# Kernel optimization log

Hardware: AMD Instinct MI355X
Metric: run time of the kernel (lower is better)

The kernel has to match this reference:

```python
import jax, jax.numpy as jnp
import numpy as np

SEQ_LEN = 2048
D_MODEL = 1024
K = 32
B = 16
CP = K * (K + 1) // 2  # 528


def _spectral_filters(seq_len: int, k: int) -> np.ndarray:
    # Hankel matrix Z_ij = 2 / ((i+j)^3 - (i+j)), 1-indexed
    e = np.arange(1, seq_len + 1, dtype=np.float64)
    ipj = e[:, None] + e[None, :]
    Z = 2.0 / (ipj ** 3 - ipj)
    sigma, phi = np.linalg.eigh(Z)
    sk = np.clip(sigma[-k:], 1e-9, None)
    return (phi[:, -k:] * sk ** 0.25).astype(np.float32)


# static upper-triangular index pattern and sqrt(2) off-diagonal scaling
_IU0, _IU1 = np.triu_indices(K)
_SCALE = np.where(_IU0 == _IU1, 1.0, np.sqrt(2.0)).astype(np.float32)


def setup_inputs() -> dict:
    key = jax.random.key(0)
    ks = jax.random.split(key, 8)
    filters = jnp.asarray(_spectral_filters(SEQ_LEN, K))
    x = jax.random.normal(ks[0], (B, SEQ_LEN, D_MODEL), dtype=jnp.float32)
    pre_w = jax.random.normal(ks[1], (SEQ_LEN, D_MODEL), dtype=jnp.float32) / np.sqrt(D_MODEL)
    pre_b = jnp.zeros((SEQ_LEN,), dtype=jnp.float32)
    qp_w = jax.random.normal(ks[2], (CP, K), dtype=jnp.float32) / np.sqrt(K)
    qp_b = jnp.zeros((CP,), dtype=jnp.float32)
    o_w = jax.random.normal(ks[3], (D_MODEL, CP), dtype=jnp.float32) / np.sqrt(CP)
    o_b = jnp.zeros((D_MODEL,), dtype=jnp.float32)
    decay = jnp.ones((SEQ_LEN,), dtype=jnp.float32)
    return {
        'x': x,
        'pre_w': pre_w, 'pre_b': pre_b,
        'q_filters': filters,          # learnable copy
        'k_filters': filters,          # fixed buffer copy
        'qp_w': qp_w, 'qp_b': qp_b,
        'o_w': o_w, 'o_b': o_b,
        'decay': decay,
    }


def reference(x, pre_w, pre_b, q_filters, k_filters, qp_w, qp_b, o_w, o_b, decay):
    # pre_proj: (B,T,d_model) -> (B,T,seq_len)
    x_proj = x @ pre_w.T + pre_b
    # spectral projections onto top-K filters: (B,T,K)
    Q = jnp.einsum('bti,ik->btk', x_proj, q_filters)
    Q = Q @ qp_w.T + qp_b                      # (B,T,CP)
    V = jnp.einsum('bti,ik->btk', x_proj, k_filters)
    # symmetric outer product compressed to upper triangle, off-diag * sqrt(2)
    iu0 = jnp.asarray(_IU0)
    iu1 = jnp.asarray(_IU1)
    scale = jnp.asarray(_SCALE)
    Z = V[..., iu0] * V[..., iu1] * scale      # (B,T,CP), avoids (B,T,K,K)
    Z = Z * decay[None, :, None]
    H = jnp.cumsum(Z, axis=1)                  # causal state accumulation
    Y = Q * H
    return Y @ o_w.T + o_b                     # (B,T,d_model)
```

## Files before the change

### kernel.cpp

```cpp
#include <hip/hip_runtime.h>
#include <hip/hip_bf16.h>
#include <math.h>

#define T_SEQ   2048
#define DM      1024
#define KF      32
#define BATCH   16
#define CPDIM   528
#define KPAD    544
#define YSTR    552
#define MROWS   (BATCH * T_SEQ)
#define NCHUNK  32
#define TCHUNK  64

typedef __bf16 bf16x8 __attribute__((ext_vector_type(8)));
typedef float f32x4 __attribute__((ext_vector_type(4)));
typedef unsigned uint2v __attribute__((ext_vector_type(2)));

__device__ __forceinline__ unsigned packsplit(float v) {
  unsigned u = __float_as_uint(v);
  unsigned h = (u + 0x7fffu + ((u >> 16) & 1u)) & 0xffff0000u;
  float rr = v - __uint_as_float(h);
  return h | (__float_as_uint(rr) >> 16);
}

__device__ __forceinline__ unsigned short f2bf(float f) {
  unsigned u = __float_as_uint(f);
  return (unsigned short)((u + 0x7fffu + ((u >> 16) & 1u)) >> 16);
}
__device__ __forceinline__ float bf2f(unsigned short h) {
  return __uint_as_float((unsigned)h << 16);
}

__device__ __forceinline__ void gload16(const void* g, void* l) {
  __builtin_amdgcn_global_load_lds(
      (const __attribute__((address_space(1))) unsigned*)g,
      (__attribute__((address_space(3))) unsigned*)l, 16, 0, 0);
}

__global__ __launch_bounds__(256) void k_fold_part(const float* __restrict__ pre_w,
                                                   const float* __restrict__ qf,
                                                   const float* __restrict__ kfil,
                                                   float* __restrict__ Wp) {
  const int sc = blockIdx.x;
  const int it = blockIdx.y;
  const int s0 = sc * 64, i0 = it * 64;
  const int tid = threadIdx.x;
  __shared__ float fs[64][64];
  __shared__ float ps[64][64];
  for (int idx = tid; idx < 4096; idx += 256) {
    const int s = idx >> 6, c = idx & 63;
    fs[s][c] = (c < KF) ? qf[(s0 + s) * KF + c] : kfil[(s0 + s) * KF + c - KF];
    ps[s][c] = pre_w[(size_t)(s0 + s) * DM + i0 + c];
  }
  __syncthreads();
  const int i = tid & 63;
  const int kb = tid >> 6;
  float acc[16] = {};
  for (int s = 0; s < 64; ++s) {
    const float pv = ps[s][i];
    const float4 f0 = *reinterpret_cast<const float4*>(&fs[s][kb * 16 + 0]);
    const float4 f1 = *reinterpret_cast<const float4*>(&fs[s][kb * 16 + 4]);
    const float4 f2 = *reinterpret_cast<const float4*>(&fs[s][kb * 16 + 8]);
    const float4 f3 = *reinterpret_cast<const float4*>(&fs[s][kb * 16 + 12]);
    acc[0]  = fmaf(pv, f0.x, acc[0]);  acc[1]  = fmaf(pv, f0.y, acc[1]);
    acc[2]  = fmaf(pv, f0.z, acc[2]);  acc[3]  = fmaf(pv, f0.w, acc[3]);
    acc[4]  = fmaf(pv, f1.x, acc[4]);  acc[5]  = fmaf(pv, f1.y, acc[5]);
    acc[6]  = fmaf(pv, f1.z, acc[6]);  acc[7]  = fmaf(pv, f1.w, acc[7]);
    acc[8]  = fmaf(pv, f2.x, acc[8]);  acc[9]  = fmaf(pv, f2.y, acc[9]);
    acc[10] = fmaf(pv, f2.z, acc[10]); acc[11] = fmaf(pv, f2.w, acc[11]);
    acc[12] = fmaf(pv, f3.x, acc[12]); acc[13] = fmaf(pv, f3.y, acc[13]);
    acc[14] = fmaf(pv, f3.z, acc[14]); acc[15] = fmaf(pv, f3.w, acc[15]);
  }
#pragma unroll
  for (int j = 0; j < 16; ++j)
    Wp[((size_t)sc * 64 + kb * 16 + j) * DM + i0 + i] = acc[j];
}

__global__ __launch_bounds__(256) void k_foldred_bias(const float* __restrict__ Wp,
                                                      const float* __restrict__ pre_b,
                                                      const float* __restrict__ qf,
                                                      const float* __restrict__ kfil,
                                                      unsigned short* __restrict__ Wt_hi,
                                                      unsigned short* __restrict__ Wt_lo,
                                                      float* __restrict__ bias64) {
  if (blockIdx.x == 256) {
    __shared__ float part[4][64];
    const int k = threadIdx.x & 63;
    const int q = threadIdx.x >> 6;
    float acc = 0.f;
    for (int s = q * 512; s < (q + 1) * 512; ++s) {
      const float fv = (k < KF) ? qf[s * KF + k] : kfil[s * KF + k - KF];
      acc = fmaf(pre_b[s], fv, acc);
    }
    part[q][k] = acc;
    __syncthreads();
    if (threadIdx.x < 64)
      bias64[threadIdx.x] = part[0][k] + part[1][k] + part[2][k] + part[3][k];
    return;
  }
  const int idx = blockIdx.x * 256 + threadIdx.x;
  float acc = 0.f;
#pragma unroll
  for (int sc = 0; sc < NCHUNK; ++sc)
    acc += Wp[(size_t)sc * 64 * DM + idx];
  const unsigned pk = packsplit(acc);
  Wt_hi[idx] = (unsigned short)(pk >> 16);
  Wt_lo[idx] = (unsigned short)(pk & 0xffffu);
}

__global__ __launch_bounds__(512) void k_q0v_cs(const float* __restrict__ x,
                                                const unsigned short* __restrict__ Wt_hi,
                                                const unsigned short* __restrict__ Wt_lo,
                                                const float* __restrict__ bias64,
                                                const float* __restrict__ decay,
                                                float* __restrict__ Q0V,
                                                float* __restrict__ S) {
  __shared__ float Xs[3][64 * 32];
  __shared__ unsigned short Wh[3][64 * 32];
  __shared__ unsigned short Wl[3][64 * 32];
  __shared__ float vs2[64 * 32];
  __shared__ float dec2[64];
  const int tid = threadIdx.x;
  const int m0 = blockIdx.x * 64;
  const int ph = blockIdx.x & 31;
  const int w = tid >> 6, l = tid & 63;
  const int g = l >> 4, r = l & 15;
  const int wr = w & 3, wh = w >> 2;

  f32x4 acc[2] = {};

  auto kcol = [&](int i) { return ((i + ph) & 31) * 32; };

  auto stage = [&](int buf, int k0) {
    {
      const int row = tid >> 3, sl = tid & 7;
      const int col4 = (sl ^ (row & 7)) * 4;
      gload16(&x[(size_t)(m0 + row) * DM + k0 + col4], &Xs[buf][tid * 4]);
    }
    {
      const int c2 = tid & 255;
      const int row = c2 >> 2, sl = c2 & 3;
      const int colh = (sl ^ ((row >> 1) & 3)) * 8;
      unsigned short* dst = (tid < 256) ? &Wh[buf][c2 * 8] : &Wl[buf][c2 * 8];
      const unsigned short* src = (tid < 256) ? &Wt_hi[(size_t)row * DM + k0 + colh]
                                              : &Wt_lo[(size_t)row * DM + k0 + colh];
      gload16(src, dst);
    }
  };

  auto compute = [&](int cur) {
    const int arow = wr * 16 + r;
    const int sx = (2 * g) ^ (arow & 7);
    const int sy = (2 * g + 1) ^ (arow & 7);
    const f32x4 pX = *reinterpret_cast<const f32x4*>(&Xs[cur][arow * 32 + sx * 4]);
    const f32x4 pY = *reinterpret_cast<const f32x4*>(&Xs[cur][arow * 32 + sy * 4]);
    unsigned pk[8];
#pragma unroll
    for (int e = 0; e < 4; ++e) { pk[e] = packsplit(pX[e]); pk[4 + e] = packsplit(pY[e]); }
    union { unsigned u[4]; bf16x8 v; } ah, al;
#pragma unroll
    for (int j = 0; j < 4; ++j) {
      ah.u[j] = (pk[2 * j] >> 16) | (pk[2 * j + 1] & 0xffff0000u);
      al.u[j] = (pk[2 * j] & 0xffffu) | (pk[2 * j + 1] << 16);
    }
    bf16x8 bh[2], bl[2];
#pragma unroll
    for (int nb = 0; nb < 2; ++nb) {
      const int brow = (wh * 2 + nb) * 16 + r;
      const int bs = g ^ ((brow >> 1) & 3);
      const int off = brow * 32 + bs * 8;
      bh[nb] = *reinterpret_cast<const bf16x8*>(&Wh[cur][off]);
      bl[nb] = *reinterpret_cast<const bf16x8*>(&Wl[cur][off]);
    }
#pragma unroll
    for (int nb = 0; nb < 2; ++nb) {
      acc[nb] = __builtin_amdgcn_mfma_f32_16x16x32_bf16(bh[nb], ah.v, acc[nb], 0, 0, 0);
      acc[nb] = __builtin_amdgcn_mfma_f32_16x16x32_bf16(bh[nb], al.v, acc[nb], 0, 0, 0);
      acc[nb] = __builtin_amdgcn_mfma_f32_16x16x32_bf16(bl[nb], ah.v, acc[nb], 0, 0, 0);
    }
  };

  if (tid < 64) dec2[tid] = decay[(m0 & 2047) + tid];

  stage(0, kcol(0));
  stage(1, kcol(1));

  for (int base = 0; base < 30; base += 3) {
#pragma unroll
    for (int sub = 0; sub < 3; ++sub) {
      const int it = base + sub;
      asm volatile("s_waitcnt vmcnt(2)" ::: "memory");
      __builtin_amdgcn_s_barrier();
      __builtin_amdgcn_sched_barrier(0);
      stage((sub + 2) % 3, kcol(it + 2));
      compute(sub);
    }
  }
  asm volatile("s_waitcnt vmcnt(2)" ::: "memory");
  __builtin_amdgcn_s_barrier();
  __builtin_amdgcn_sched_barrier(0);
  compute(0);
  asm volatile("s_waitcnt vmcnt(0)" ::: "memory");
  __builtin_amdgcn_s_barrier();
  __builtin_amdgcn_sched_barrier(0);
  compute(1);

  const int trow = wr * 16 + r;
  const int row_o = m0 + trow;
#pragma unroll
  for (int nb = 0; nb < 2; ++nb) {
    const int n = wh * 2 + nb;
    const int col_o = n * 16 + g * 4;
    const float4 bb = *reinterpret_cast<const float4*>(&bias64[col_o]);
    float4 v;
    v.x = acc[nb][0] + bb.x; v.y = acc[nb][1] + bb.y;
    v.z = acc[nb][2] + bb.z; v.w = acc[nb][3] + bb.w;
    *reinterpret_cast<float4*>(&Q0V[(size_t)row_o * 64 + col_o]) = v;
    if (n >= 2)
      *reinterpret_cast<float4*>(&vs2[trow * 32 + (n - 2) * 16 + g * 4]) = v;
  }
  __syncthreads();

  const int b = m0 >> 11, ch = (m0 & 2047) >> 6;
#pragma unroll
  for (int pass = 0; pass < 2; ++pass) {
    const int c = tid + pass * 512;
    if (c < CPDIM) {
      int i = 0, rem = c;
      while (rem >= KF - i) { rem -= KF - i; ++i; }
      const int j = i + rem;
      const float sc = (i == j) ? 1.0f : 1.41421356237309515f;
      float h = 0.f;
#pragma unroll 4
      for (int t = 0; t < TCHUNK; ++t)
        h = fmaf(vs2[t * KF + i] * vs2[t * KF + j], dec2[t], h);
      S[(size_t)(b * NCHUNK + ch) * CPDIM + c] = h * sc;
    }
  }
}

__global__ __launch_bounds__(576) void k_scanchunks(float* __restrict__ S) {
  const int b = blockIdx.x;
  const int c = threadIdx.x;
  if (c >= CPDIM) return;
  float v[NCHUNK];
#pragma unroll
  for (int ch = 0; ch < NCHUNK; ++ch)
    v[ch] = S[(size_t)(b * NCHUNK + ch) * CPDIM + c];
  float run = 0.f;
#pragma unroll
  for (int ch = 0; ch < NCHUNK; ++ch) {
    S[(size_t)(b * NCHUNK + ch) * CPDIM + c] = run;
    run += v[ch];
  }
}

#define NB_OWB  (DM * KPAD / 256)
#define NB_QPW  (KPAD * KF / 256)
__global__ __launch_bounds__(256) void k_prep(const float* __restrict__ ow,
                                              const float* __restrict__ qp_w,
                                              const float* __restrict__ qp_b,
                                              unsigned short* __restrict__ owb,
                                              unsigned short* __restrict__ qpw_hi,
                                              unsigned short* __restrict__ qpw_lo,
                                              float* __restrict__ qpb_pad) {
  const int bx = blockIdx.x;
  if (bx < NB_OWB) {
    const int idx = bx * 256 + threadIdx.x;
    const int n = idx / KPAD, k = idx - n * KPAD;
    owb[idx] = (k < CPDIM) ? f2bf(ow[(size_t)n * CPDIM + k]) : (unsigned short)0;
  } else if (bx < NB_OWB + NB_QPW) {
    const int idx = (bx - NB_OWB) * 256 + threadIdx.x;
    const int c = idx >> 5;
    unsigned pk = 0;
    if (c < CPDIM) pk = packsplit(qp_w[idx]);
    qpw_hi[idx] = (unsigned short)(pk >> 16);
    qpw_lo[idx] = (unsigned short)(pk & 0xffffu);
  } else {
    for (int c = threadIdx.x; c < KPAD; c += 256)
      qpb_pad[c] = (c < CPDIM) ? qp_b[c] : 0.f;
  }
}

__global__ __launch_bounds__(1024, 4) void k_out_fused(const float* __restrict__ Q0V,
                                                       const float* __restrict__ S,
                                                       const unsigned short* __restrict__ qpw_hi,
                                                       const unsigned short* __restrict__ qpw_lo,
                                                       const float* __restrict__ qpb_pad,
                                                       const float* __restrict__ decay,
                                                       const unsigned short* __restrict__ owb,
                                                       const float* __restrict__ ob,
                                                       float* __restrict__ out) {
  __shared__ unsigned short Ylds[64 * YSTR];
  const int tid = threadIdx.x;
  const int m0 = blockIdx.x * 64;
  const int b = m0 >> 11, ch = (m0 & 2047) >> 6;
  const int t0 = m0 & 2047;
  const int wv = tid >> 6, l = tid & 63;
  const int g = l >> 4, r = l & 15;

  {
    bf16x8 qah[4], qal[4];
#pragma unroll
    for (int m = 0; m < 4; ++m) {
      const int t = m * 16 + r;
      const f32x4 x0 = *reinterpret_cast<const f32x4*>(&Q0V[(size_t)(m0 + t) * 64 + g * 8]);
      const f32x4 x1 = *reinterpret_cast<const f32x4*>(&Q0V[(size_t)(m0 + t) * 64 + g * 8 + 4]);
      unsigned pk[8];
#pragma unroll
      for (int e = 0; e < 4; ++e) { pk[e] = packsplit(x0[e]); pk[4 + e] = packsplit(x1[e]); }
      union { unsigned u[4]; bf16x8 v; } hh, ll;
#pragma unroll
      for (int j = 0; j < 4; ++j) {
        hh.u[j] = (pk[2 * j] >> 16) | (pk[2 * j + 1] & 0xffff0000u);
        ll.u[j] = (pk[2 * j] & 0xffffu) | (pk[2 * j + 1] << 16);
      }
      qah[m] = hh.v; qal[m] = ll.v;
    }
    for (int nt = wv; nt < KPAD / 16; nt += 16) {
      const int crow = nt * 16 + r;
      const bf16x8 bh = *reinterpret_cast<const bf16x8*>(&qpw_hi[crow * KF + g * 8]);
      const bf16x8 bl = *reinterpret_cast<const bf16x8*>(&qpw_lo[crow * KF + g * 8]);
      const int cbase = nt * 16 + g * 4;
      const float4 qb4 = *reinterpret_cast<const float4*>(&qpb_pad[cbase]);
      f32x4 a[4];
#pragma unroll
      for (int m = 0; m < 4; ++m) { a[m][0] = qb4.x; a[m][1] = qb4.y; a[m][2] = qb4.z; a[m][3] = qb4.w; }
#pragma unroll
      for (int m = 0; m < 4; ++m) {
        a[m] = __builtin_amdgcn_mfma_f32_16x16x32_bf16(bh, qah[m], a[m], 0, 0, 0);
        a[m] = __builtin_amdgcn_mfma_f32_16x16x32_bf16(bh, qal[m], a[m], 0, 0, 0);
        a[m] = __builtin_amdgcn_mfma_f32_16x16x32_bf16(bl, qah[m], a[m], 0, 0, 0);
      }
#pragma unroll
      for (int m = 0; m < 4; ++m) {
        const int t = m * 16 + r;
        union { unsigned short s[4]; unsigned u[2]; } pk4;
#pragma unroll
        for (int j = 0; j < 4; ++j) pk4.s[j] = f2bf(a[m][j]);
        *reinterpret_cast<uint2v*>(&Ylds[t * YSTR + cbase]) = uint2v{pk4.u[0], pk4.u[1]};
      }
    }
  }
  __syncthreads();

  if (tid < CPDIM) {
    const int c = tid;
    int i = 0, rem = c;
    while (rem >= KF - i) { rem -= KF - i; ++i; }
    const int j = i + rem;
    const float sc = (i == j) ? 1.0f : 1.41421356237309515f;
    const float* vrow = &Q0V[(size_t)m0 * 64 + 32];
    float h = S[(size_t)(b * NCHUNK + ch) * CPDIM + c];
#pragma unroll 8
    for (int t = 0; t < TCHUNK; ++t) {
      const float vi = vrow[t * 64 + i];
      const float vj = vrow[t * 64 + j];
      h = fmaf(vi * vj * sc, decay[t0 + t], h);
      const float qv = bf2f(Ylds[t * YSTR + c]);
      Ylds[t * YSTR + c] = f2bf(qv * h);
    }
  }
  __syncthreads();

  f32x4 acc[4][4] = {};
  bf16x8 bfA[4], bfB[4];

  auto loadB = [&](bf16x8 (&dst)[4], int ks) {
    const int kh = ks * 32 + g * 8;
#pragma unroll
    for (int n = 0; n < 4; ++n)
      dst[n] = *reinterpret_cast<const bf16x8*>(&owb[(size_t)(wv * 64 + n * 16 + r) * KPAD + kh]);
  };
  auto step = [&](const bf16x8 (&bc)[4], int ks) {
    const int kh = ks * 32 + g * 8;
    bf16x8 af[4];
#pragma unroll
    for (int m = 0; m < 4; ++m)
      af[m] = *reinterpret_cast<const bf16x8*>(&Ylds[(m * 16 + r) * YSTR + kh]);
#pragma unroll
    for (int m = 0; m < 4; ++m)
#pragma unroll
      for (int n = 0; n < 4; ++n)
        acc[m][n] = __builtin_amdgcn_mfma_f32_16x16x32_bf16(bc[n], af[m], acc[m][n], 0, 0, 0);
  };

  loadB(bfA, 0);
#pragma unroll
  for (int ks = 0; ks < 16; ks += 2) {
    loadB(bfB, ks + 1);
    step(bfA, ks);
    loadB(bfA, ks + 2);
    step(bfB, ks + 1);
  }
  step(bfA, 16);

#pragma unroll
  for (int m = 0; m < 4; ++m) {
    const int row_o = m0 + m * 16 + r;
#pragma unroll
    for (int n = 0; n < 4; ++n) {
      const int col_o = wv * 64 + n * 16 + g * 4;
      const float4 bb = *reinterpret_cast<const float4*>(&ob[col_o]);
      float4 v;
      v.x = acc[m][n][0] + bb.x; v.y = acc[m][n][1] + bb.y;
      v.z = acc[m][n][2] + bb.z; v.w = acc[m][n][3] + bb.w;
      *reinterpret_cast<float4*>(&out[(size_t)row_o * DM + col_o]) = v;
    }
  }
}

extern "C" void kernel_launch(void* const* d_in, const int* in_sizes, int n_in,
                              void* d_out, int out_size, void* d_ws, size_t ws_size,
                              hipStream_t stream) {
  const float* x      = (const float*)d_in[0];
  const float* pre_w  = (const float*)d_in[1];
  const float* pre_b  = (const float*)d_in[2];
  const float* q_filt = (const float*)d_in[3];
  const float* k_filt = (const float*)d_in[4];
  const float* qp_w   = (const float*)d_in[5];
  const float* qp_b   = (const float*)d_in[6];
  const float* o_w    = (const float*)d_in[7];
  const float* o_b    = (const float*)d_in[8];
  const float* decay  = (const float*)d_in[9];
  float* out = (float*)d_out;

  char* ws = (char*)d_ws;
  unsigned short* Wt_hi = (unsigned short*)(ws);
  unsigned short* Wt_lo = (unsigned short*)(ws + 131072);
  float*    bias64 = (float*)(ws + 262144);
  float*    Q0V    = (float*)(ws + 262400);
  float*    S      = (float*)(ws + 8651008);
  unsigned short* owb = (unsigned short*)(ws + 9732352);
  unsigned short* qpw_hi = (unsigned short*)(ws + 10846464);
  unsigned short* qpw_lo = (unsigned short*)(ws + 10881280);
  float*    qpb_pad = (float*)(ws + 10916096);
  float*    Wp     = (float*)(ws + 16777216);

  k_fold_part<<<dim3(NCHUNK, 16), dim3(256), 0, stream>>>(pre_w, q_filt, k_filt, Wp);
  k_foldred_bias<<<dim3(257), dim3(256), 0, stream>>>(Wp, pre_b, q_filt, k_filt, Wt_hi, Wt_lo, bias64);
  k_q0v_cs<<<dim3(MROWS / 64), dim3(512), 0, stream>>>(x, Wt_hi, Wt_lo, bias64, decay, Q0V, S);
  k_scanchunks<<<dim3(BATCH), dim3(576), 0, stream>>>(S);
  k_prep<<<dim3(NB_OWB + NB_QPW + 1), dim3(256), 0, stream>>>(o_w, qp_w, qp_b, owb, qpw_hi, qpw_lo, qpb_pad);
  k_out_fused<<<dim3(MROWS / 64), dim3(1024), 0, stream>>>(Q0V, S, qpw_hi, qpw_lo, qpb_pad, decay, owb, o_b, out);
}
```

Measured before the change: 171.7 us.

## Replace triple-buffered k-loop with four large bulk-loaded LDS stages

The projection kernel's 32-step, triple-buffered global-to-LDS pipeline is replaced with four coarse stages. Each stage bulk-loads a 256-wide slice of x and both bf16 weight halves into much larger shared buffers, synchronizes, then runs eight MFMA steps. The aim is fewer barriers and more bytes in flight per load. In exchange, loads no longer overlap compute, shared memory per block grows to about 136KB, which limits occupancy, and the per-block k-rotation that spread accesses across blocks is dropped.

```diff
diff --git a/kernel.cpp b/kernel.cpp
--- a/kernel.cpp
+++ b/kernel.cpp
@@ -116,45 +116,25 @@
                                                 const float* __restrict__ decay,
                                                 float* __restrict__ Q0V,
                                                 float* __restrict__ S) {
-  __shared__ float Xs[3][64 * 32];
-  __shared__ unsigned short Wh[3][64 * 32];
-  __shared__ unsigned short Wl[3][64 * 32];
+  __shared__ float XsBig[64 * 256];
+  __shared__ unsigned short WhBig[8 * 64 * 32];
+  __shared__ unsigned short WlBig[8 * 64 * 32];
   __shared__ float vs2[64 * 32];
   __shared__ float dec2[64];
   const int tid = threadIdx.x;
   const int m0 = blockIdx.x * 64;
-  const int ph = blockIdx.x & 31;
   const int w = tid >> 6, l = tid & 63;
   const int g = l >> 4, r = l & 15;
   const int wr = w & 3, wh = w >> 2;
 
   f32x4 acc[2] = {};
 
-  auto kcol = [&](int i) { return ((i + ph) & 31) * 32; };
-
-  auto stage = [&](int buf, int k0) {
-    {
-      const int row = tid >> 3, sl = tid & 7;
-      const int col4 = (sl ^ (row & 7)) * 4;
-      gload16(&x[(size_t)(m0 + row) * DM + k0 + col4], &Xs[buf][tid * 4]);
-    }
-    {
-      const int c2 = tid & 255;
-      const int row = c2 >> 2, sl = c2 & 3;
-      const int colh = (sl ^ ((row >> 1) & 3)) * 8;
-      unsigned short* dst = (tid < 256) ? &Wh[buf][c2 * 8] : &Wl[buf][c2 * 8];
-      const unsigned short* src = (tid < 256) ? &Wt_hi[(size_t)row * DM + k0 + colh]
-                                              : &Wt_lo[(size_t)row * DM + k0 + colh];
-      gload16(src, dst);
-    }
-  };
-
-  auto compute = [&](int cur) {
+  auto compute = [&](int kk) {
     const int arow = wr * 16 + r;
     const int sx = (2 * g) ^ (arow & 7);
     const int sy = (2 * g + 1) ^ (arow & 7);
-    const f32x4 pX = *reinterpret_cast<const f32x4*>(&Xs[cur][arow * 32 + sx * 4]);
-    const f32x4 pY = *reinterpret_cast<const f32x4*>(&Xs[cur][arow * 32 + sy * 4]);
+    const f32x4 pX = *reinterpret_cast<const f32x4*>(&XsBig[arow * 256 + kk * 32 + sx * 4]);
+    const f32x4 pY = *reinterpret_cast<const f32x4*>(&XsBig[arow * 256 + kk * 32 + sy * 4]);
     unsigned pk[8];
 #pragma unroll
     for (int e = 0; e < 4; ++e) { pk[e] = packsplit(pX[e]); pk[4 + e] = packsplit(pY[e]); }
@@ -169,9 +149,9 @@
     for (int nb = 0; nb < 2; ++nb) {
       const int brow = (wh * 2 + nb) * 16 + r;
       const int bs = g ^ ((brow >> 1) & 3);
-      const int off = brow * 32 + bs * 8;
-      bh[nb] = *reinterpret_cast<const bf16x8*>(&Wh[cur][off]);
-      bl[nb] = *reinterpret_cast<const bf16x8*>(&Wl[cur][off]);
+      const int off = kk * 2048 + brow * 32 + bs * 8;
+      bh[nb] = *reinterpret_cast<const bf16x8*>(&WhBig[off]);
+      bl[nb] = *reinterpret_cast<const bf16x8*>(&WlBig[off]);
     }
 #pragma unroll
     for (int nb = 0; nb < 2; ++nb) {
@@ -183,28 +163,28 @@
 
   if (tid < 64) dec2[tid] = decay[(m0 & 2047) + tid];
 
-  stage(0, kcol(0));
-  stage(1, kcol(1));
-
-  for (int base = 0; base < 30; base += 3) {
-#pragma unroll
-    for (int sub = 0; sub < 3; ++sub) {
-      const int it = base + sub;
-      asm volatile("s_waitcnt vmcnt(2)" ::: "memory");
-      __builtin_amdgcn_s_barrier();
-      __builtin_amdgcn_sched_barrier(0);
-      stage((sub + 2) % 3, kcol(it + 2));
-      compute(sub);
-    }
-  }
-  asm volatile("s_waitcnt vmcnt(2)" ::: "memory");
-  __builtin_amdgcn_s_barrier();
-  __builtin_amdgcn_sched_barrier(0);
-  compute(0);
-  asm volatile("s_waitcnt vmcnt(0)" ::: "memory");
-  __builtin_amdgcn_s_barrier();
-  __builtin_amdgcn_sched_barrier(0);
-  compute(1);
+  for (int s = 0; s < 4; ++s) {
+    __syncthreads();
+#pragma unroll
+    for (int q = 0; q < 8; ++q) {
+      const int c = q * 512 + tid;
+      const int row = c >> 6, l6 = c & 63;
+      const int cq = (l6 & 56) | ((l6 & 7) ^ (row & 7));
+      gload16(&x[(size_t)(m0 + row) * DM + s * 256 + cq * 4], &XsBig[c * 4]);
+    }
+#pragma unroll
+    for (int q = 0; q < 4; ++q) {
+      const int c = q * 512 + tid;
+      const int kk = c >> 8, row = (c >> 2) & 63, sl = c & 3;
+      const int colh = kk * 32 + (sl ^ ((row >> 1) & 3)) * 8;
+      gload16(&Wt_hi[(size_t)row * DM + s * 256 + colh], &WhBig[c * 8]);
+      gload16(&Wt_lo[(size_t)row * DM + s * 256 + colh], &WlBig[c * 8]);
+    }
+    __syncthreads();
+#pragma unroll
+    for (int kk = 0; kk < 8; ++kk)
+      compute(kk);
+  }
 
   const int trow = wr * 16 + r;
   const int row_o = m0 + trow;
```

Measured after the change: 196.5 us. 1.14x slower.
